# Kernel optimization log

Measured on AMD Instinct MI355X. Metric: run time of the kernel, lower is better.

## Reference

```python
import jax, jax.numpy as jnp
import numpy as np

C_ATOM, C_Z, N_HEADS = 512, 64, 16
HEAD_DIM = C_ATOM // N_HEADS
EPS = 1e-5


def _layernorm(x, gamma, beta):
    mu = jnp.mean(x, axis=-1, keepdims=True)
    var = jnp.mean(jnp.square(x - mu), axis=-1, keepdims=True)
    return (x - mu) * jax.lax.rsqrt(var + EPS) * gamma + beta


def _adaln(x, cond, gamma, beta, pw, pb):
    # cond: [B, C] -> scale/shift: [B, 1, C]
    ss = cond @ pw.T + pb  # [B, 2C]
    scale, shift = jnp.split(ss[:, None, :], 2, axis=-1)
    return _layernorm(x, gamma, beta) * (1.0 + scale) + shift


def setup_inputs() -> dict:
    key = jax.random.key(0)
    ks = jax.random.split(key, 20)
    B, L = 2, 1024
    s = 1.0 / np.sqrt(C_ATOM)
    inp = {
        "x": jax.random.normal(ks[0], (B, L, C_ATOM), jnp.float32),
        "pair": jax.random.normal(ks[1], (B, L, L, C_Z), jnp.float32),
        "time_cond": jax.random.normal(ks[2], (B, C_ATOM), jnp.float32),
        "ln1_g": jnp.ones((C_ATOM,), jnp.float32),
        "ln1_b": jnp.zeros((C_ATOM,), jnp.float32),
        "ada1_w": jax.random.normal(ks[3], (2 * C_ATOM, C_ATOM), jnp.float32) * 0.02,
        "ada1_b": jnp.zeros((2 * C_ATOM,), jnp.float32),
        "wq": jax.random.normal(ks[4], (C_ATOM, C_ATOM), jnp.float32) * s,
        "wk": jax.random.normal(ks[5], (C_ATOM, C_ATOM), jnp.float32) * s,
        "wv": jax.random.normal(ks[6], (C_ATOM, C_ATOM), jnp.float32) * s,
        "w_pair": jax.random.normal(ks[7], (N_HEADS, C_Z), jnp.float32) * (1.0 / np.sqrt(C_Z)),
        "wo": jax.random.normal(ks[8], (C_ATOM, C_ATOM), jnp.float32) * s,
        "bo": jnp.zeros((C_ATOM,), jnp.float32),
        "ln2_g": jnp.ones((C_ATOM,), jnp.float32),
        "ln2_b": jnp.zeros((C_ATOM,), jnp.float32),
        "ada2_w": jax.random.normal(ks[9], (2 * C_ATOM, C_ATOM), jnp.float32) * 0.02,
        "ada2_b": jnp.zeros((2 * C_ATOM,), jnp.float32),
        "w1": jax.random.normal(ks[10], (4 * C_ATOM, C_ATOM), jnp.float32) * s,
        "b1": jnp.zeros((4 * C_ATOM,), jnp.float32),
        "w2": jax.random.normal(ks[11], (C_ATOM, 4 * C_ATOM), jnp.float32) * (1.0 / np.sqrt(4 * C_ATOM)),
        "b2": jnp.zeros((C_ATOM,), jnp.float32),
    }
    return inp


def reference(x, pair, time_cond, ln1_g, ln1_b, ada1_w, ada1_b, wq, wk, wv,
              w_pair, wo, bo, ln2_g, ln2_b, ada2_w, ada2_b, w1, b1, w2, b2):
    B, L, C = x.shape
    h = _adaln(x, time_cond, ln1_g, ln1_b, ada1_w, ada1_b)
    q = (h @ wq.T).reshape(B, L, N_HEADS, HEAD_DIM)
    k = (h @ wk.T).reshape(B, L, N_HEADS, HEAD_DIM)
    v = (h @ wv.T).reshape(B, L, N_HEADS, HEAD_DIM)
    attn = jnp.einsum('bihd,bjhd->bhij', q, k) / np.sqrt(HEAD_DIM)
    attn = attn + jnp.einsum('bijc,hc->bhij', pair, w_pair)  # additive pair bias
    attn = jax.nn.softmax(attn, axis=-1)
    out = jnp.einsum('bhij,bjhd->bihd', attn, v).reshape(B, L, C)
    x = x + out @ wo.T + bo
    h2 = _adaln(x, time_cond, ln2_g, ln2_b, ada2_w, ada2_b)
    ffn = jax.nn.gelu(h2 @ w1.T + b1, approximate=False) @ w2.T + b2
    return x + ffn
```

## Files before the change

### kernel.cpp

```cpp
#include <hip/hip_runtime.h>
#include <math.h>

typedef unsigned short u16;
typedef __attribute__((ext_vector_type(8))) short bf16x8;
typedef __attribute__((ext_vector_type(4))) short s16x4;
typedef __attribute__((ext_vector_type(4))) float f32x4;

__device__ __forceinline__ u16 f2bf(float f) {
  union { float f; unsigned u; } v; v.f = f;
  unsigned r = v.u + 0x7FFFu + ((v.u >> 16) & 1u);
  return (u16)(r >> 16);
}
__device__ __forceinline__ float bf2f(u16 h) {
  union { unsigned u; float f; } v; v.u = ((unsigned)h) << 16; return v.f;
}
__device__ __forceinline__ void gload_lds16(const void* g, void* l) {
  __builtin_amdgcn_global_load_lds((const __attribute__((address_space(1))) void*)g,
                                   (__attribute__((address_space(3))) void*)l, 16, 0, 0);
}

__global__ __launch_bounds__(256) void k_pre(
    const float* __restrict__ wq, const float* __restrict__ wk,
    const float* __restrict__ wv, const float* __restrict__ wo,
    const float* __restrict__ w1, const float* __restrict__ w2,
    u16* __restrict__ qkvw, u16* __restrict__ wo_bf,
    u16* __restrict__ w1_bf, u16* __restrict__ w2_bf,
    const float* __restrict__ tc,
    const float* __restrict__ wa, const float* __restrict__ ba,
    const float* __restrict__ wb, const float* __restrict__ bb,
    float* __restrict__ ss1, float* __restrict__ ss2) {
  if (blockIdx.x < 3072) {
    int i = (blockIdx.x * 256 + threadIdx.x) * 4;
    const float* s; u16* d;
    if (i < 786432) {
      d = qkvw + i;
      if (i < 262144) s = wq + i;
      else if (i < 524288) s = wk + (i - 262144);
      else s = wv + (i - 524288);
    } else if (i < 1048576) { s = wo + (i - 786432); d = wo_bf + (i - 786432); }
    else if (i < 2097152)   { s = w1 + (i - 1048576); d = w1_bf + (i - 1048576); }
    else                    { s = w2 + (i - 2097152); d = w2_bf + (i - 2097152); }
    float4 v = *(const float4*)s;
    s16x4 o;
    o[0] = (short)f2bf(v.x); o[1] = (short)f2bf(v.y);
    o[2] = (short)f2bf(v.z); o[3] = (short)f2bf(v.w);
    *(s16x4*)d = o;
  } else {
    int wv_ = (blockIdx.x - 3072) * 4 + (threadIdx.x >> 6);
    int l = threadIdx.x & 63;
    int which = wv_ >> 11;
    int rem = wv_ & 2047;
    int b = rem >> 10;
    int row = rem & 1023;
    const float* w = which ? wb : wa;
    const float4* t4 = (const float4*)(tc + b * 512);
    const float4* w4 = (const float4*)(w + (size_t)row * 512);
    float s = 0.f;
#pragma unroll
    for (int q = 0; q < 2; ++q) {
      float4 a = t4[l * 2 + q], c = w4[l * 2 + q];
      s += a.x * c.x + a.y * c.y + a.z * c.z + a.w * c.w;
    }
#pragma unroll
    for (int m = 32; m; m >>= 1) s += __shfl_xor(s, m);
    if (l == 0) {
      float bias = (which ? bb : ba)[row];
      (which ? ss2 : ss1)[b * 1024 + row] = s + bias;
    }
  }
}

__global__ __launch_bounds__(256) void k_adaln(const float* __restrict__ x,
    const float* __restrict__ g, const float* __restrict__ be,
    const float* __restrict__ ss, u16* __restrict__ out) {
  int r = blockIdx.x * 4 + (threadIdx.x >> 6);
  int l = threadIdx.x & 63;
  int b = r >> 10;
  const float4* x4 = (const float4*)(x + (size_t)r * 512);
  float4 v0 = x4[l * 2], v1 = x4[l * 2 + 1];
  float s = v0.x + v0.y + v0.z + v0.w + v1.x + v1.y + v1.z + v1.w;
  float s2 = v0.x*v0.x + v0.y*v0.y + v0.z*v0.z + v0.w*v0.w
           + v1.x*v1.x + v1.y*v1.y + v1.z*v1.z + v1.w*v1.w;
#pragma unroll
  for (int m = 32; m; m >>= 1) { s += __shfl_xor(s, m); s2 += __shfl_xor(s2, m); }
  float mu = s * (1.f / 512.f);
  float var = s2 * (1.f / 512.f) - mu * mu;
  float rstd = rsqrtf(var + 1e-5f);
  int c = l * 8;
  float4 g0 = *(const float4*)(g + c),  g1 = *(const float4*)(g + c + 4);
  float4 e0 = *(const float4*)(be + c), e1 = *(const float4*)(be + c + 4);
  const float* sb = ss + b * 1024;
  float4 sc0 = *(const float4*)(sb + c),       sc1 = *(const float4*)(sb + c + 4);
  float4 sh0 = *(const float4*)(sb + 512 + c), sh1 = *(const float4*)(sb + 512 + c + 4);
  float xe[8] = {v0.x,v0.y,v0.z,v0.w,v1.x,v1.y,v1.z,v1.w};
  float gg[8] = {g0.x,g0.y,g0.z,g0.w,g1.x,g1.y,g1.z,g1.w};
  float ee[8] = {e0.x,e0.y,e0.z,e0.w,e1.x,e1.y,e1.z,e1.w};
  float sc[8] = {sc0.x,sc0.y,sc0.z,sc0.w,sc1.x,sc1.y,sc1.z,sc1.w};
  float sh[8] = {sh0.x,sh0.y,sh0.z,sh0.w,sh1.x,sh1.y,sh1.z,sh1.w};
  bf16x8 o;
#pragma unroll
  for (int e = 0; e < 8; ++e) {
    float hv = (xe[e] - mu) * rstd * gg[e] + ee[e];
    float res = hv * (1.f + sc[e]) + sh[e];
    o[e] = (short)f2bf(res);
  }
  *(bf16x8*)(out + (size_t)r * 512 + c) = o;
}

template<int MODE, int BM, int BN>
__device__ __forceinline__ void gemm_body(
    int bxn, int bxm,
    const u16* __restrict__ A, const u16* __restrict__ Bw,
    int M, int N, int K,
    u16* __restrict__ obf, float* __restrict__ of,
    const float* __restrict__ cb, const float* __restrict__ add_,
    float qscale) {
  constexpr int FM = BM / 32, FN = BN / 32;
  constexpr int WM = BM / 2,  WN = BN / 2;
  __shared__ u16 la[BM * 64];
  __shared__ u16 lb[BN * 64];
  const int tid = threadIdx.x;
  const int l = tid & 63, w = tid >> 6;
  const int wr = w >> 1, wc = w & 1;
  const int m0 = bxm * BM, n0 = bxn * BN;
  f32x4 acc[FM][FN];
  const f32x4 fz = {0.f, 0.f, 0.f, 0.f};
#pragma unroll
  for (int m = 0; m < FM; ++m)
#pragma unroll
    for (int n = 0; n < FN; ++n) acc[m][n] = fz;
  const int nkt = K >> 6;
  for (int kt = 0; kt < nkt; ++kt) {
    const int k0 = kt * 64;
    __syncthreads();
#pragma unroll
    for (int r2 = 0; r2 < BM / 32; ++r2) {
      unsigned e = r2 * 256 + tid;
      unsigned row = e >> 3, ch = (e & 7) ^ (row & 7);
      gload_lds16(A + (size_t)(m0 + row) * K + k0 + ch * 8, la + (e & ~63u) * 8);
    }
#pragma unroll
    for (int r2 = 0; r2 < BN / 32; ++r2) {
      unsigned e = r2 * 256 + tid;
      unsigned row = e >> 3, ch = (e & 7) ^ (row & 7);
      gload_lds16(Bw + (size_t)(n0 + row) * K + k0 + ch * 8, lb + (e & ~63u) * 8);
    }
    __syncthreads();
#pragma unroll
    for (int kk = 0; kk < 2; ++kk) {
      bf16x8 af[FM], bfr[FN];
#pragma unroll
      for (int m = 0; m < FM; ++m) {
        int R = wr * WM + m * 16 + (l & 15);
        int ch = (kk * 4 + (l >> 4)) ^ (R & 7);
        af[m] = *(const bf16x8*)(la + R * 64 + ch * 8);
      }
#pragma unroll
      for (int n = 0; n < FN; ++n) {
        int R = wc * WN + n * 16 + (l & 15);
        int ch = (kk * 4 + (l >> 4)) ^ (R & 7);
        bfr[n] = *(const bf16x8*)(lb + R * 64 + ch * 8);
      }
#pragma unroll
      for (int m = 0; m < FM; ++m)
#pragma unroll
        for (int n = 0; n < FN; ++n)
          acc[m][n] = __builtin_amdgcn_mfma_f32_16x16x32_bf16(af[m], bfr[n], acc[m][n], 0, 0, 0);
    }
  }
  const int rb  = m0 + wr * WM + ((l >> 4) * 4);
  const int cb0 = n0 + wc * WN + (l & 15);
#pragma unroll
  for (int m = 0; m < FM; ++m)
#pragma unroll
    for (int n = 0; n < FN; ++n) {
      int gcol = cb0 + n * 16;
#pragma unroll
      for (int j = 0; j < 4; ++j) {
        int grow = rb + m * 16 + j;
        float v = acc[m][n][j];
        if (MODE == 0) {
          float scv = (gcol < 512) ? qscale : 1.f;
          obf[(size_t)grow * N + gcol] = f2bf(v * scv);
        } else if (MODE == 1) {
          of[(size_t)grow * N + gcol] = v + cb[gcol] + add_[(size_t)grow * N + gcol];
        } else {
          float t = v + cb[gcol];
          float ge = 0.5f * t * (1.f + erff(t * 0.70710678118654752f));
          obf[(size_t)grow * N + gcol] = f2bf(ge);
        }
      }
    }
}

template<int MODE, int BM, int BN>
__global__ __launch_bounds__(256) void k_gemm(
    const u16* __restrict__ A, const u16* __restrict__ Bw,
    int M, int N, int K,
    u16* __restrict__ obf, float* __restrict__ of,
    const float* __restrict__ cb, const float* __restrict__ add_,
    float qscale) {
  gemm_body<MODE, BM, BN>(blockIdx.x, blockIdx.y, A, Bw, M, N, K, obf, of, cb, add_, qscale);
}

__device__ __forceinline__ void bias_body(int blk, const float* __restrict__ pair,
    const float* __restrict__ wp, u16* __restrict__ bias) {
  const int tid = threadIdx.x, l = tid & 63, w = tid >> 6;
  bf16x8 bfrag[2];
  {
    const float* wb = wp + (l & 15) * 64 + (l >> 4) * 8;
#pragma unroll
    for (int kk = 0; kk < 2; ++kk) {
      float4 w0 = *(const float4*)(wb + kk * 32);
      float4 w1 = *(const float4*)(wb + kk * 32 + 4);
      bf16x8 bb;
      bb[0] = (short)f2bf(w0.x); bb[1] = (short)f2bf(w0.y);
      bb[2] = (short)f2bf(w0.z); bb[3] = (short)f2bf(w0.w);
      bb[4] = (short)f2bf(w1.x); bb[5] = (short)f2bf(w1.y);
      bb[6] = (short)f2bf(w1.z); bb[7] = (short)f2bf(w1.w);
      bfrag[kk] = bb;
    }
  }
  const size_t m_base = (size_t)blk * 1024 + w * 256;
  const f32x4 fz = {0.f, 0.f, 0.f, 0.f};
#pragma unroll 4
  for (int f = 0; f < 16; ++f) {
    size_t row = m_base + f * 16 + (l & 15);
    const float* pr = pair + row * 64 + (l >> 4) * 8;
    float4 p0 = *(const float4*)(pr);
    float4 p1 = *(const float4*)(pr + 4);
    float4 p2 = *(const float4*)(pr + 32);
    float4 p3 = *(const float4*)(pr + 36);
    bf16x8 a0, a1;
    a0[0] = (short)f2bf(p0.x); a0[1] = (short)f2bf(p0.y);
    a0[2] = (short)f2bf(p0.z); a0[3] = (short)f2bf(p0.w);
    a0[4] = (short)f2bf(p1.x); a0[5] = (short)f2bf(p1.y);
    a0[6] = (short)f2bf(p1.z); a0[7] = (short)f2bf(p1.w);
    a1[0] = (short)f2bf(p2.x); a1[1] = (short)f2bf(p2.y);
    a1[2] = (short)f2bf(p2.z); a1[3] = (short)f2bf(p2.w);
    a1[4] = (short)f2bf(p3.x); a1[5] = (short)f2bf(p3.y);
    a1[6] = (short)f2bf(p3.z); a1[7] = (short)f2bf(p3.w);
    f32x4 acc = __builtin_amdgcn_mfma_f32_16x16x32_bf16(a0, bfrag[0], fz, 0, 0, 0);
    acc = __builtin_amdgcn_mfma_f32_16x16x32_bf16(a1, bfrag[1], acc, 0, 0, 0);
    size_t m0c = m_base + f * 16 + (l >> 4) * 4;
    size_t b = m0c >> 20;
    size_t ij = m0c & 1048575;
    u16* dst = bias + (((b << 4) + (l & 15)) << 20) + ij;
    s16x4 ov;
    ov[0] = (short)f2bf(acc[0]); ov[1] = (short)f2bf(acc[1]);
    ov[2] = (short)f2bf(acc[2]); ov[3] = (short)f2bf(acc[3]);
    *(s16x4*)dst = ov;
  }
}

__global__ __launch_bounds__(256) void k_mega(
    const u16* __restrict__ h_bf, const u16* __restrict__ qkvw,
    u16* __restrict__ qkv_bf, float qscale,
    const float* __restrict__ pair, const float* __restrict__ wp,
    u16* __restrict__ bias) {
  if (blockIdx.x < 192) {
    gemm_body<0, 128, 128>(blockIdx.x % 12, blockIdx.x / 12,
        h_bf, qkvw, 2048, 1536, 512, qkv_bf, nullptr, nullptr, nullptr, qscale);
  } else {
    bias_body(blockIdx.x - 192, pair, wp, bias);
  }
}

__global__ __launch_bounds__(256) void k_attn(const u16* __restrict__ qkv,
    const u16* __restrict__ bias, u16* __restrict__ ob) {
  __shared__ u16 kl[64 * 40];
  __shared__ u16 vt[32 * 64];
  __shared__ u16 bl[64 * 64];
  __shared__ u16 pl[4][16 * 64];
  __shared__ float cw[4][16];
  __shared__ float lw[4][16];
  const int tid = threadIdx.x, l = tid & 63, w = tid >> 6;
  const int g = l >> 4;
  const int i0 = blockIdx.x * 64;
  const int h  = blockIdx.y;
  const int b  = blockIdx.z;
  const u16* base = qkv + (size_t)b * 1024 * 1536 + h * 32;
  const int ib = w * 16 + (l & 15);
  const bf16x8 qb = *(const bf16x8*)(base + (size_t)(i0 + ib) * 1536 + g * 8);
  float mr = -1e30f, lr = 0.f;
  f32x4 oa[2];
  const f32x4 fz = {0.f, 0.f, 0.f, 0.f};
  oa[0] = fz; oa[1] = fz;
  const size_t bbase = ((size_t)(b * 16 + h) * 1024 + (size_t)i0) * 1024;
  u16* plw = &pl[w][0];
  for (int jt = 0; jt < 16; ++jt) {
    const int j0 = jt * 64;
    __syncthreads();
    {
      int row = tid >> 2, d8 = (tid & 3) * 8;
      *(bf16x8*)(kl + row * 40 + d8) = *(const bf16x8*)(base + 512 + (size_t)(j0 + row) * 1536 + d8);
      bf16x8 vv = *(const bf16x8*)(base + 1024 + (size_t)(j0 + row) * 1536 + d8);
#pragma unroll
      for (int e = 0; e < 8; ++e)
        vt[(d8 + e) * 64 + (row ^ (e << 3))] = (u16)vv[e];
      int il = tid >> 2, jl = (tid & 3) * 16;
      int v_ = (il & 7) << 3;
      const u16* bs = bias + bbase + (size_t)il * 1024 + j0 + jl;
      *(bf16x8*)(bl + il * 64 + (jl ^ v_))       = *(const bf16x8*)bs;
      *(bf16x8*)(bl + il * 64 + ((jl + 8) ^ v_)) = *(const bf16x8*)(bs + 8);
    }
    __syncthreads();
    f32x4 s[4];
#pragma unroll
    for (int jf = 0; jf < 4; ++jf) {
      int R = jf * 16 + (l & 15);
      bf16x8 ak = *(const bf16x8*)(kl + R * 40 + g * 8);
      s[jf] = __builtin_amdgcn_mfma_f32_16x16x32_bf16(ak, qb, fz, 0, 0, 0);
    }
#pragma unroll
    for (int jf = 0; jf < 4; ++jf) {
      int c = jf * 16 + g * 4;
      s16x4 bv = *(const s16x4*)(bl + ib * 64 + (c ^ ((ib & 7) << 3)));
#pragma unroll
      for (int r = 0; r < 4; ++r) s[jf][r] += bf2f((u16)bv[r]);
    }
    float rm = s[0][0];
#pragma unroll
    for (int jf = 0; jf < 4; ++jf)
#pragma unroll
      for (int r = 0; r < 4; ++r) rm = fmaxf(rm, s[jf][r]);
    rm = fmaxf(rm, __shfl_xor(rm, 16));
    rm = fmaxf(rm, __shfl_xor(rm, 32));
    float mn = fmaxf(mr, rm);
    float corr = __expf(mr - mn);
    float p[4][4];
    float rs = 0.f;
#pragma unroll
    for (int jf = 0; jf < 4; ++jf)
#pragma unroll
      for (int r = 0; r < 4; ++r) { p[jf][r] = __expf(s[jf][r] - mn); rs += p[jf][r]; }
    rs += __shfl_xor(rs, 16);
    rs += __shfl_xor(rs, 32);
    lr = lr * corr + rs;
    mr = mn;
    if (l < 16) cw[w][l] = corr;
#pragma unroll
    for (int jf = 0; jf < 4; ++jf) {
      s16x4 pv;
#pragma unroll
      for (int r = 0; r < 4; ++r) pv[r] = (short)f2bf(p[jf][r]);
      int c = jf * 16 + g * 4;
      *(s16x4*)(plw + (l & 15) * 64 + (c ^ (((l & 15) & 7) << 3))) = pv;
    }
    float cr0 = cw[w][g * 4 + 0], cr1 = cw[w][g * 4 + 1];
    float cr2 = cw[w][g * 4 + 2], cr3 = cw[w][g * 4 + 3];
#pragma unroll
    for (int n = 0; n < 2; ++n) {
      oa[n][0] *= cr0; oa[n][1] *= cr1; oa[n][2] *= cr2; oa[n][3] *= cr3;
    }
#pragma unroll
    for (int kk = 0; kk < 2; ++kk) {
      int ip = l & 15;
      bf16x8 pa = *(const bf16x8*)(plw + ip * 64 + ((kk * 32 + g * 8) ^ ((ip & 7) << 3)));
#pragma unroll
      for (int n = 0; n < 2; ++n) {
        int dp = n * 16 + (l & 15);
        bf16x8 vb = *(const bf16x8*)(vt + dp * 64 + ((kk * 32 + g * 8) ^ ((dp & 7) << 3)));
        oa[n] = __builtin_amdgcn_mfma_f32_16x16x32_bf16(pa, vb, oa[n], 0, 0, 0);
      }
    }
  }
  if (l < 16) lw[w][l] = lr;
  float lv0 = lw[w][g * 4 + 0], lv1 = lw[w][g * 4 + 1];
  float lv2 = lw[w][g * 4 + 2], lv3 = lw[w][g * 4 + 3];
#pragma unroll
  for (int n = 0; n < 2; ++n) {
    float lvr[4] = {lv0, lv1, lv2, lv3};
#pragma unroll
    for (int r = 0; r < 4; ++r) {
      float v = oa[n][r] / lvr[r];
      ob[(size_t)(b * 1024 + i0 + w * 16 + g * 4 + r) * 512 + h * 32 + n * 16 + (l & 15)] = f2bf(v);
    }
  }
}

extern "C" void kernel_launch(void* const* d_in, const int* in_sizes, int n_in,
                              void* d_out, int out_size, void* d_ws, size_t ws_size,
                              hipStream_t stream) {
  const float* x    = (const float*)d_in[0];
  const float* pair = (const float*)d_in[1];
  const float* tc   = (const float*)d_in[2];
  const float* ln1g = (const float*)d_in[3];
  const float* ln1b = (const float*)d_in[4];
  const float* a1w  = (const float*)d_in[5];
  const float* a1b  = (const float*)d_in[6];
  const float* wq   = (const float*)d_in[7];
  const float* wk   = (const float*)d_in[8];
  const float* wv   = (const float*)d_in[9];
  const float* wp   = (const float*)d_in[10];
  const float* wo   = (const float*)d_in[11];
  const float* bo   = (const float*)d_in[12];
  const float* ln2g = (const float*)d_in[13];
  const float* ln2b = (const float*)d_in[14];
  const float* a2w  = (const float*)d_in[15];
  const float* a2b  = (const float*)d_in[16];
  const float* w1   = (const float*)d_in[17];
  const float* b1   = (const float*)d_in[18];
  const float* w2   = (const float*)d_in[19];
  const float* b2   = (const float*)d_in[20];
  float* out = (float*)d_out;

  char* ws = (char*)d_ws;
  size_t off = 0;
  auto alloc = [&](size_t bytes) {
    size_t cur = off;
    off += (bytes + 255) & ~(size_t)255;
    return (void*)(ws + cur);
  };
  float* ss1    = (float*)alloc(2 * 1024 * 4);
  float* ss2    = (float*)alloc(2 * 1024 * 4);
  u16*   qkvw   = (u16*)alloc((size_t)1536 * 512 * 2);
  u16*   wo_bf  = (u16*)alloc((size_t)512 * 512 * 2);
  u16*   w1_bf  = (u16*)alloc((size_t)2048 * 512 * 2);
  u16*   w2_bf  = (u16*)alloc((size_t)512 * 2048 * 2);
  u16*   h_bf   = (u16*)alloc((size_t)2048 * 512 * 2);
  u16*   qkv_bf = (u16*)alloc((size_t)2048 * 1536 * 2);
  u16*   o_bf   = (u16*)alloc((size_t)2048 * 512 * 2);
  u16*   h2_bf  = (u16*)alloc((size_t)2048 * 512 * 2);
  float* xmid   = (float*)alloc((size_t)2048 * 512 * 4);
  u16*   mid_bf = (u16*)alloc((size_t)2048 * 2048 * 2);
  u16*   bias_bf= (u16*)alloc((size_t)2 * 16 * 1024 * 1024 * 2);
  (void)ws_size; (void)in_sizes; (void)n_in; (void)out_size;

  k_pre<<<4096, 256, 0, stream>>>(wq, wk, wv, wo, w1, w2,
                                  qkvw, wo_bf, w1_bf, w2_bf,
                                  tc, a1w, a1b, a2w, a2b, ss1, ss2);

  k_adaln<<<512, 256, 0, stream>>>(x, ln1g, ln1b, ss1, h_bf);

  k_mega<<<2240, 256, 0, stream>>>(h_bf, qkvw, qkv_bf, 0.17677669529663687f,
                                   pair, wp, bias_bf);

  k_attn<<<dim3(16, 16, 2), 256, 0, stream>>>(qkv_bf, bias_bf, o_bf);

  k_gemm<1, 64, 64><<<dim3(8, 32), 256, 0, stream>>>(o_bf, wo_bf, 2048, 512, 512,
      nullptr, xmid, bo, x, 1.f);

  k_adaln<<<512, 256, 0, stream>>>(xmid, ln2g, ln2b, ss2, h2_bf);

  k_gemm<2, 64, 128><<<dim3(16, 32), 256, 0, stream>>>(h2_bf, w1_bf, 2048, 2048, 512,
      mid_bf, nullptr, b1, nullptr, 1.f);

  k_gemm<1, 64, 64><<<dim3(8, 32), 256, 0, stream>>>(mid_bf, w2_bf, 2048, 512, 2048,
      nullptr, out, b2, xmid, 1.f);
}
```

Before: 239.0 us.

## Fuse pair-bias projection into attention kernel, removing bias buffer round-trip

Attention becomes a single kernel that computes the pair-bias projection on the fly with MFMA from the fp32 pair tensor and keeps it in shared memory. Each 512-thread block covers 16 query rows across all 16 heads, two heads per wave. This removes the write and re-read of the large bf16 bias tensor, and the QKV GEMM now runs as its own launch. In exchange the grid shrinks to 128 blocks, which may leave CUs idle. K fragments are also read straight from global memory and V is transposed per wave, which adds redundant loads.

```diff
diff --git a/kernel.cpp b/kernel.cpp
--- a/kernel.cpp
+++ b/kernel.cpp
@@ -203,179 +203,157 @@
   gemm_body<MODE, BM, BN>(blockIdx.x, blockIdx.y, A, Bw, M, N, K, obf, of, cb, add_, qscale);
 }
 
-__device__ __forceinline__ void bias_body(int blk, const float* __restrict__ pair,
-    const float* __restrict__ wp, u16* __restrict__ bias) {
+__global__ __launch_bounds__(512) void k_fab2(const u16* __restrict__ qkv,
+    const float* __restrict__ pair, const float* __restrict__ wp,
+    u16* __restrict__ ob) {
+  __shared__ u16 vt[8][64 * 64];
+  __shared__ u16 bt[16][16 * 68];
+  __shared__ u16 pl[8][2][16 * 64];
   const int tid = threadIdx.x, l = tid & 63, w = tid >> 6;
-  bf16x8 bfrag[2];
-  {
-    const float* wb = wp + (l & 15) * 64 + (l >> 4) * 8;
-#pragma unroll
-    for (int kk = 0; kk < 2; ++kk) {
-      float4 w0 = *(const float4*)(wb + kk * 32);
-      float4 w1 = *(const float4*)(wb + kk * 32 + 4);
-      bf16x8 bb;
-      bb[0] = (short)f2bf(w0.x); bb[1] = (short)f2bf(w0.y);
-      bb[2] = (short)f2bf(w0.z); bb[3] = (short)f2bf(w0.w);
-      bb[4] = (short)f2bf(w1.x); bb[5] = (short)f2bf(w1.y);
-      bb[6] = (short)f2bf(w1.z); bb[7] = (short)f2bf(w1.w);
-      bfrag[kk] = bb;
-    }
-  }
-  const size_t m_base = (size_t)blk * 1024 + w * 256;
+  const int g = l >> 4, ln = l & 15;
+  const int i0 = blockIdx.x * 16;
+  const int b  = blockIdx.y;
+  const u16* base = qkv + (size_t)b * 1024 * 1536;
   const f32x4 fz = {0.f, 0.f, 0.f, 0.f};
-#pragma unroll 4
-  for (int f = 0; f < 16; ++f) {
-    size_t row = m_base + f * 16 + (l & 15);
-    const float* pr = pair + row * 64 + (l >> 4) * 8;
-    float4 p0 = *(const float4*)(pr);
-    float4 p1 = *(const float4*)(pr + 4);
-    float4 p2 = *(const float4*)(pr + 32);
-    float4 p3 = *(const float4*)(pr + 36);
-    bf16x8 a0, a1;
-    a0[0] = (short)f2bf(p0.x); a0[1] = (short)f2bf(p0.y);
-    a0[2] = (short)f2bf(p0.z); a0[3] = (short)f2bf(p0.w);
-    a0[4] = (short)f2bf(p1.x); a0[5] = (short)f2bf(p1.y);
-    a0[6] = (short)f2bf(p1.z); a0[7] = (short)f2bf(p1.w);
-    a1[0] = (short)f2bf(p2.x); a1[1] = (short)f2bf(p2.y);
-    a1[2] = (short)f2bf(p2.z); a1[3] = (short)f2bf(p2.w);
-    a1[4] = (short)f2bf(p3.x); a1[5] = (short)f2bf(p3.y);
-    a1[6] = (short)f2bf(p3.z); a1[7] = (short)f2bf(p3.w);
-    f32x4 acc = __builtin_amdgcn_mfma_f32_16x16x32_bf16(a0, bfrag[0], fz, 0, 0, 0);
-    acc = __builtin_amdgcn_mfma_f32_16x16x32_bf16(a1, bfrag[1], acc, 0, 0, 0);
-    size_t m0c = m_base + f * 16 + (l >> 4) * 4;
-    size_t b = m0c >> 20;
-    size_t ij = m0c & 1048575;
-    u16* dst = bias + (((b << 4) + (l & 15)) << 20) + ij;
-    s16x4 ov;
-    ov[0] = (short)f2bf(acc[0]); ov[1] = (short)f2bf(acc[1]);
-    ov[2] = (short)f2bf(acc[2]); ov[3] = (short)f2bf(acc[3]);
-    *(s16x4*)dst = ov;
-  }
-}
-
-__global__ __launch_bounds__(256) void k_mega(
-    const u16* __restrict__ h_bf, const u16* __restrict__ qkvw,
-    u16* __restrict__ qkv_bf, float qscale,
-    const float* __restrict__ pair, const float* __restrict__ wp,
-    u16* __restrict__ bias) {
-  if (blockIdx.x < 192) {
-    gemm_body<0, 128, 128>(blockIdx.x % 12, blockIdx.x / 12,
-        h_bf, qkvw, 2048, 1536, 512, qkv_bf, nullptr, nullptr, nullptr, qscale);
-  } else {
-    bias_body(blockIdx.x - 192, pair, wp, bias);
-  }
-}
-
-__global__ __launch_bounds__(256) void k_attn(const u16* __restrict__ qkv,
-    const u16* __restrict__ bias, u16* __restrict__ ob) {
-  __shared__ u16 kl[64 * 40];
-  __shared__ u16 vt[32 * 64];
-  __shared__ u16 bl[64 * 64];
-  __shared__ u16 pl[4][16 * 64];
-  __shared__ float cw[4][16];
-  __shared__ float lw[4][16];
-  const int tid = threadIdx.x, l = tid & 63, w = tid >> 6;
-  const int g = l >> 4;
-  const int i0 = blockIdx.x * 64;
-  const int h  = blockIdx.y;
-  const int b  = blockIdx.z;
-  const u16* base = qkv + (size_t)b * 1024 * 1536 + h * 32;
-  const int ib = w * 16 + (l & 15);
-  const bf16x8 qb = *(const bf16x8*)(base + (size_t)(i0 + ib) * 1536 + g * 8);
-  float mr = -1e30f, lr = 0.f;
-  f32x4 oa[2];
-  const f32x4 fz = {0.f, 0.f, 0.f, 0.f};
-  oa[0] = fz; oa[1] = fz;
-  const size_t bbase = ((size_t)(b * 16 + h) * 1024 + (size_t)i0) * 1024;
-  u16* plw = &pl[w][0];
+  bf16x8 wf[2];
+#pragma unroll
+  for (int kk = 0; kk < 2; ++kk) {
+    const float* wb = wp + ln * 64 + kk * 32 + g * 8;
+    float4 w0 = *(const float4*)(wb);
+    float4 w1 = *(const float4*)(wb + 4);
+    bf16x8 bb;
+    bb[0] = (short)f2bf(w0.x); bb[1] = (short)f2bf(w0.y);
+    bb[2] = (short)f2bf(w0.z); bb[3] = (short)f2bf(w0.w);
+    bb[4] = (short)f2bf(w1.x); bb[5] = (short)f2bf(w1.y);
+    bb[6] = (short)f2bf(w1.z); bb[7] = (short)f2bf(w1.w);
+    wf[kk] = bb;
+  }
+  bf16x8 qb[2];
+#pragma unroll
+  for (int hh = 0; hh < 2; ++hh)
+    qb[hh] = *(const bf16x8*)(base + (size_t)(i0 + ln) * 1536 + (w * 2 + hh) * 32 + g * 8);
+  float mr[2] = {-1e30f, -1e30f}, ls[2] = {0.f, 0.f};
+  f32x4 oa[2][2];
+  oa[0][0] = fz; oa[0][1] = fz; oa[1][0] = fz; oa[1][1] = fz;
   for (int jt = 0; jt < 16; ++jt) {
     const int j0 = jt * 64;
     __syncthreads();
+#pragma unroll
+    for (int ii = 0; ii < 2; ++ii) {
+      const float* prow = pair + ((size_t)(b * 1024 + i0 + w * 2 + ii) * 1024 + j0) * 64;
+#pragma unroll
+      for (int jf = 0; jf < 4; ++jf) {
+        f32x4 ab = fz;
+#pragma unroll
+        for (int kk = 0; kk < 2; ++kk) {
+          const float* pp = prow + (jf * 16 + ln) * 64 + kk * 32 + g * 8;
+          float4 p0 = *(const float4*)(pp);
+          float4 p1 = *(const float4*)(pp + 4);
+          bf16x8 pk;
+          pk[0] = (short)f2bf(p0.x); pk[1] = (short)f2bf(p0.y);
+          pk[2] = (short)f2bf(p0.z); pk[3] = (short)f2bf(p0.w);
+          pk[4] = (short)f2bf(p1.x); pk[5] = (short)f2bf(p1.y);
+          pk[6] = (short)f2bf(p1.z); pk[7] = (short)f2bf(p1.w);
+          ab = __builtin_amdgcn_mfma_f32_16x16x32_bf16(pk, wf[kk], ab, 0, 0, 0);
+        }
+        s16x4 ov;
+        ov[0] = (short)f2bf(ab[0]); ov[1] = (short)f2bf(ab[1]);
+        ov[2] = (short)f2bf(ab[2]); ov[3] = (short)f2bf(ab[3]);
+        *(s16x4*)(&bt[ln][(w * 2 + ii) * 68 + jf * 16 + g * 4]) = ov;
+      }
+    }
     {
-      int row = tid >> 2, d8 = (tid & 3) * 8;
-      *(bf16x8*)(kl + row * 40 + d8) = *(const bf16x8*)(base + 512 + (size_t)(j0 + row) * 1536 + d8);
-      bf16x8 vv = *(const bf16x8*)(base + 1024 + (size_t)(j0 + row) * 1536 + d8);
-#pragma unroll
-      for (int e = 0; e < 8; ++e)
-        vt[(d8 + e) * 64 + (row ^ (e << 3))] = (u16)vv[e];
-      int il = tid >> 2, jl = (tid & 3) * 16;
-      int v_ = (il & 7) << 3;
-      const u16* bs = bias + bbase + (size_t)il * 1024 + j0 + jl;
-      *(bf16x8*)(bl + il * 64 + (jl ^ v_))       = *(const bf16x8*)bs;
-      *(bf16x8*)(bl + il * 64 + ((jl + 8) ^ v_)) = *(const bf16x8*)(bs + 8);
+      const u16* vrow = base + (size_t)(j0 + l) * 1536 + 1024 + w * 64;
+      bf16x8 vv[8];
+#pragma unroll
+      for (int q = 0; q < 8; ++q) vv[q] = *(const bf16x8*)(vrow + q * 8);
+#pragma unroll
+      for (int q = 0; q < 8; ++q)
+#pragma unroll
+        for (int e = 0; e < 8; ++e) {
+          int d = q * 8 + e;
+          vt[w][d * 64 + (l ^ ((d & 7) << 3))] = (u16)vv[q][e];
+        }
     }
     __syncthreads();
-    f32x4 s[4];
-#pragma unroll
-    for (int jf = 0; jf < 4; ++jf) {
-      int R = jf * 16 + (l & 15);
-      bf16x8 ak = *(const bf16x8*)(kl + R * 40 + g * 8);
-      s[jf] = __builtin_amdgcn_mfma_f32_16x16x32_bf16(ak, qb, fz, 0, 0, 0);
-    }
-#pragma unroll
-    for (int jf = 0; jf < 4; ++jf) {
-      int c = jf * 16 + g * 4;
-      s16x4 bv = *(const s16x4*)(bl + ib * 64 + (c ^ ((ib & 7) << 3)));
-#pragma unroll
-      for (int r = 0; r < 4; ++r) s[jf][r] += bf2f((u16)bv[r]);
-    }
-    float rm = s[0][0];
-#pragma unroll
-    for (int jf = 0; jf < 4; ++jf)
-#pragma unroll
-      for (int r = 0; r < 4; ++r) rm = fmaxf(rm, s[jf][r]);
-    rm = fmaxf(rm, __shfl_xor(rm, 16));
-    rm = fmaxf(rm, __shfl_xor(rm, 32));
-    float mn = fmaxf(mr, rm);
-    float corr = __expf(mr - mn);
-    float p[4][4];
-    float rs = 0.f;
-#pragma unroll
-    for (int jf = 0; jf < 4; ++jf)
-#pragma unroll
-      for (int r = 0; r < 4; ++r) { p[jf][r] = __expf(s[jf][r] - mn); rs += p[jf][r]; }
-    rs += __shfl_xor(rs, 16);
-    rs += __shfl_xor(rs, 32);
-    lr = lr * corr + rs;
-    mr = mn;
-    if (l < 16) cw[w][l] = corr;
-#pragma unroll
-    for (int jf = 0; jf < 4; ++jf) {
-      s16x4 pv;
-#pragma unroll
-      for (int r = 0; r < 4; ++r) pv[r] = (short)f2bf(p[jf][r]);
-      int c = jf * 16 + g * 4;
-      *(s16x4*)(plw + (l & 15) * 64 + (c ^ (((l & 15) & 7) << 3))) = pv;
-    }
-    float cr0 = cw[w][g * 4 + 0], cr1 = cw[w][g * 4 + 1];
-    float cr2 = cw[w][g * 4 + 2], cr3 = cw[w][g * 4 + 3];
-#pragma unroll
-    for (int n = 0; n < 2; ++n) {
-      oa[n][0] *= cr0; oa[n][1] *= cr1; oa[n][2] *= cr2; oa[n][3] *= cr3;
-    }
-#pragma unroll
-    for (int kk = 0; kk < 2; ++kk) {
-      int ip = l & 15;
-      bf16x8 pa = *(const bf16x8*)(plw + ip * 64 + ((kk * 32 + g * 8) ^ ((ip & 7) << 3)));
-#pragma unroll
-      for (int n = 0; n < 2; ++n) {
-        int dp = n * 16 + (l & 15);
-        bf16x8 vb = *(const bf16x8*)(vt + dp * 64 + ((kk * 32 + g * 8) ^ ((dp & 7) << 3)));
-        oa[n] = __builtin_amdgcn_mfma_f32_16x16x32_bf16(pa, vb, oa[n], 0, 0, 0);
-      }
-    }
-  }
-  if (l < 16) lw[w][l] = lr;
-  float lv0 = lw[w][g * 4 + 0], lv1 = lw[w][g * 4 + 1];
-  float lv2 = lw[w][g * 4 + 2], lv3 = lw[w][g * 4 + 3];
-#pragma unroll
-  for (int n = 0; n < 2; ++n) {
-    float lvr[4] = {lv0, lv1, lv2, lv3};
-#pragma unroll
-    for (int r = 0; r < 4; ++r) {
-      float v = oa[n][r] / lvr[r];
-      ob[(size_t)(b * 1024 + i0 + w * 16 + g * 4 + r) * 512 + h * 32 + n * 16 + (l & 15)] = f2bf(v);
-    }
+#pragma unroll
+    for (int hh = 0; hh < 2; ++hh) {
+      const int h = w * 2 + hh;
+      f32x4 s[4];
+#pragma unroll
+      for (int jf = 0; jf < 4; ++jf) {
+        bf16x8 ak = *(const bf16x8*)(base + (size_t)(j0 + jf * 16 + ln) * 1536 + 512 + h * 32 + g * 8);
+        s[jf] = __builtin_amdgcn_mfma_f32_16x16x32_bf16(ak, qb[hh], fz, 0, 0, 0);
+      }
+#pragma unroll
+      for (int jf = 0; jf < 4; ++jf) {
+        s16x4 bv = *(const s16x4*)(&bt[h][ln * 68 + jf * 16 + g * 4]);
+        s[jf][0] += bf2f((u16)bv[0]);
+        s[jf][1] += bf2f((u16)bv[1]);
+        s[jf][2] += bf2f((u16)bv[2]);
+        s[jf][3] += bf2f((u16)bv[3]);
+      }
+      float rm = s[0][0];
+#pragma unroll
+      for (int jf = 0; jf < 4; ++jf)
+#pragma unroll
+        for (int r = 0; r < 4; ++r) rm = fmaxf(rm, s[jf][r]);
+      rm = fmaxf(rm, __shfl_xor(rm, 16));
+      rm = fmaxf(rm, __shfl_xor(rm, 32));
+      float mn = fmaxf(mr[hh], rm);
+      float corr = __expf(mr[hh] - mn);
+      float p[4][4];
+      float rs = 0.f;
+#pragma unroll
+      for (int jf = 0; jf < 4; ++jf)
+#pragma unroll
+        for (int r = 0; r < 4; ++r) { p[jf][r] = __expf(s[jf][r] - mn); rs += p[jf][r]; }
+      rs += __shfl_xor(rs, 16);
+      rs += __shfl_xor(rs, 32);
+      ls[hh] = ls[hh] * corr + rs;
+      mr[hh] = mn;
+      u16* plw = &pl[w][hh][0];
+#pragma unroll
+      for (int jf = 0; jf < 4; ++jf) {
+        s16x4 pv;
+        pv[0] = (short)f2bf(p[jf][0]); pv[1] = (short)f2bf(p[jf][1]);
+        pv[2] = (short)f2bf(p[jf][2]); pv[3] = (short)f2bf(p[jf][3]);
+        *(s16x4*)(plw + ln * 64 + ((jf * 16 + g * 4) ^ ((ln & 7) << 3))) = pv;
+      }
+      float cr[4];
+#pragma unroll
+      for (int r = 0; r < 4; ++r) cr[r] = __shfl(corr, g * 4 + r, 16);
+#pragma unroll
+      for (int nf = 0; nf < 2; ++nf) {
+        oa[hh][nf][0] *= cr[0]; oa[hh][nf][1] *= cr[1];
+        oa[hh][nf][2] *= cr[2]; oa[hh][nf][3] *= cr[3];
+      }
+#pragma unroll
+      for (int kk = 0; kk < 2; ++kk) {
+        bf16x8 pa = *(const bf16x8*)(plw + ln * 64 + ((kk * 32 + g * 8) ^ ((ln & 7) << 3)));
+#pragma unroll
+        for (int nf = 0; nf < 2; ++nf) {
+          int dp = hh * 32 + nf * 16 + ln;
+          bf16x8 vb = *(const bf16x8*)(&vt[w][dp * 64 + ((kk * 32 + g * 8) ^ ((dp & 7) << 3))]);
+          oa[hh][nf] = __builtin_amdgcn_mfma_f32_16x16x32_bf16(pa, vb, oa[hh][nf], 0, 0, 0);
+        }
+      }
+    }
+  }
+#pragma unroll
+  for (int hh = 0; hh < 2; ++hh) {
+    const int h = w * 2 + hh;
+    float lv[4];
+#pragma unroll
+    for (int r = 0; r < 4; ++r) lv[r] = __shfl(ls[hh], g * 4 + r, 16);
+#pragma unroll
+    for (int nf = 0; nf < 2; ++nf)
+#pragma unroll
+      for (int r = 0; r < 4; ++r) {
+        int m = g * 4 + r;
+        float v = oa[hh][nf][r] / lv[r];
+        ob[(size_t)(b * 1024 + i0 + m) * 512 + h * 32 + nf * 16 + ln] = f2bf(v);
+      }
   }
 }
 
@@ -424,7 +402,6 @@
   u16*   h2_bf  = (u16*)alloc((size_t)2048 * 512 * 2);
   float* xmid   = (float*)alloc((size_t)2048 * 512 * 4);
   u16*   mid_bf = (u16*)alloc((size_t)2048 * 2048 * 2);
-  u16*   bias_bf= (u16*)alloc((size_t)2 * 16 * 1024 * 1024 * 2);
   (void)ws_size; (void)in_sizes; (void)n_in; (void)out_size;
 
   k_pre<<<4096, 256, 0, stream>>>(wq, wk, wv, wo, w1, w2,
@@ -433,10 +410,10 @@
 
   k_adaln<<<512, 256, 0, stream>>>(x, ln1g, ln1b, ss1, h_bf);
 
-  k_mega<<<2240, 256, 0, stream>>>(h_bf, qkvw, qkv_bf, 0.17677669529663687f,
-                                   pair, wp, bias_bf);
-
-  k_attn<<<dim3(16, 16, 2), 256, 0, stream>>>(qkv_bf, bias_bf, o_bf);
+  k_gemm<0, 128, 128><<<dim3(12, 16), 256, 0, stream>>>(h_bf, qkvw, 2048, 1536, 512,
+      qkv_bf, nullptr, nullptr, nullptr, 0.17677669529663687f);
+
+  k_fab2<<<dim3(64, 2), 512, 0, stream>>>(qkv_bf, pair, wp, o_bf);
 
   k_gemm<1, 64, 64><<<dim3(8, 32), 256, 0, stream>>>(o_bf, wo_bf, 2048, 512, 512,
       nullptr, xmid, bo, x, 1.f);
```

After: 340.0 us. 1.42x slower.
